# Performance work log

Hardware: AMD Instinct MI355X
Metric: run time of the kernel (lower is better)

The kernel has to match this reference:

```python
import jax, jax.numpy as jnp
import numpy as np

V, E, H, W, S, T, B = 10000, 256, 512, 256, 512, 128, 64


def setup_inputs() -> dict:
    key = jax.random.key(0)
    ks = jax.random.split(key, 17)
    def rn(k, shape, s=0.08):
        return jax.random.normal(k, shape, jnp.float32) * s
    return {
        "tokens": jax.random.randint(ks[0], (B, S), 0, V),
        "dec_h0": jax.random.normal(ks[1], (B, H), jnp.float32),
        "emb_table": rn(ks[2], (V, E), 1.0),
        "enc_Wih": rn(ks[3], (4 * H, E)),
        "enc_Whh": rn(ks[4], (4 * H, H)),
        "enc_bih": rn(ks[5], (4 * H,)),
        "enc_bhh": rn(ks[6], (4 * H,)),
        "dec_Wih": rn(ks[7], (4 * H, E)),
        "dec_Whh": rn(ks[8], (4 * H, H)),
        "dec_bih": rn(ks[9], (4 * H,)),
        "dec_bhh": rn(ks[10], (4 * H,)),
        "W1_w": rn(ks[11], (W, H)),
        "W1_b": rn(ks[12], (W,)),
        "W2_w": rn(ks[13], (W, H)),
        "W2_b": rn(ks[14], (W,)),
        "vt_w": rn(ks[15], (1, W)),
        "vt_b": rn(ks[16], (1,)),
    }


def _lstm_cell(x, h, c, Wih, Whh, bih, bhh):
    # PyTorch gate order: input, forget, cell(g), output
    gates = x @ Wih.T + h @ Whh.T + bih + bhh
    i, f, g, o = jnp.split(gates, 4, axis=-1)
    c = jax.nn.sigmoid(f) * c + jax.nn.sigmoid(i) * jnp.tanh(g)
    h = jax.nn.sigmoid(o) * jnp.tanh(c)
    return h, c


def reference(tokens, dec_h0, emb_table, enc_Wih, enc_Whh, enc_bih, enc_bhh,
              dec_Wih, dec_Whh, dec_bih, dec_bhh, W1_w, W1_b, W2_w, W2_b,
              vt_w, vt_b):
    emb = emb_table[tokens]                       # [B,S,E]
    x_sbe = jnp.swapaxes(emb, 0, 1)               # [S,B,E] time-major
    bsz = tokens.shape[0]
    h0 = jnp.zeros((bsz, enc_Whh.shape[1]), emb.dtype)

    def enc_step(carry, x):
        h, c = carry
        h, c = _lstm_cell(x, h, c, enc_Wih, enc_Whh, enc_bih, enc_bhh)
        return (h, c), h

    _, enc_states = jax.lax.scan(enc_step, (h0, h0), x_sbe)   # [S,B,H]

    # W1(encoder_states) is constant across decoder steps -> hoist it
    blend1 = enc_states @ W1_w.T + W1_b            # [S,B,W]
    c0 = enc_states[-1]                            # original uses last enc state as cell init
    dec_in = jnp.zeros((bsz, emb_table.shape[1]), emb.dtype)  # never updated in original

    def dec_step(carry, _):
        h, c = carry
        h, c = _lstm_cell(dec_in, h, c, dec_Wih, dec_Whh, dec_bih, dec_bhh)
        blend2 = h @ W2_w.T + W2_b                 # [B,W]
        u = (jnp.tanh(blend1 + blend2[None]) @ vt_w.T)[..., 0] + vt_b[0]  # [S,B]
        logp = jax.nn.log_softmax(u.T, axis=1)     # [B,S], softmax over seq positions
        return (h, c), logp

    _, probs = jax.lax.scan(dec_step, (dec_h0, c0), None, length=T)  # [T,B,S]
    return jnp.swapaxes(probs, 0, 1)               # [B,T,S]
```

## Files before the change

### kernel.cpp

```cpp
#include <hip/hip_runtime.h>
#include <hip/hip_bf16.h>
#include <cstdint>
#include <cstddef>

typedef __bf16 bf16_t;
typedef __bf16 bf16x8 __attribute__((ext_vector_type(8)));
typedef float  f32x4  __attribute__((ext_vector_type(4)));

#define NB 64
#define NS 512
#define NTD 128
#define NE 256
#define NH 512
#define NG 2048
#define NW 256

#define HSTEP_DW 16384u

__device__ __forceinline__ float sigm_f(float x) { return 1.f / (1.f + __expf(-x)); }
__device__ __forceinline__ float tanh_f(float x) {
  float e = __expf(2.f * x);
  return 1.f - 2.f / (e + 1.f);
}
__device__ __forceinline__ float bits2f(uint32_t b16) {
  uint32_t u = b16 << 16;
  return __builtin_bit_cast(float, u);
}
__device__ __forceinline__ uint32_t packh(float a, float b) {
  uint16_t lo = __builtin_bit_cast(uint16_t, (bf16_t)a);
  uint16_t hi = __builtin_bit_cast(uint16_t, (bf16_t)b);
  return (uint32_t)lo | ((uint32_t)hi << 16);
}
__device__ __forceinline__ uint32_t aload(const uint32_t* p) {
  return __hip_atomic_load(p, __ATOMIC_RELAXED, __HIP_MEMORY_SCOPE_AGENT);
}
__device__ __forceinline__ uint64_t aload64(const uint64_t* p) {
  return __hip_atomic_load(p, __ATOMIC_RELAXED, __HIP_MEMORY_SCOPE_AGENT);
}
__device__ __forceinline__ void astore(uint32_t* p, uint32_t v) {
  __hip_atomic_store(p, v, __ATOMIC_RELAXED, __HIP_MEMORY_SCOPE_AGENT);
}
__device__ __forceinline__ void astoref(float* p, float v) {
  __hip_atomic_store((uint32_t*)p, __builtin_bit_cast(uint32_t, v),
                     __ATOMIC_RELAXED, __HIP_MEMORY_SCOPE_AGENT);
}
__device__ __forceinline__ float aloadf(const float* p) {
  return __builtin_bit_cast(float, aload((const uint32_t*)p));
}

__global__ __launch_bounds__(256) void pack_b(const float* __restrict__ src,
                                              bf16_t* __restrict__ dst,
                                              int N, int K) {
  int idx = blockIdx.x * 256 + threadIdx.x;
  if (idx >= N * K) return;
  int n = idx / K, k = idx - n * K;
  int lane = (((k & 31) >> 3) << 4) | (n & 15);
  size_t o = ((((size_t)(n >> 4) * (K >> 5)) + (k >> 5)) * 64 + lane) * 8 + (k & 7);
  dst[o] = (bf16_t)src[idx];
}

__global__ __launch_bounds__(256) void gather_emb(const int* __restrict__ tokens,
                                                  const float* __restrict__ table,
                                                  bf16_t* __restrict__ embfrag) {
  int idx = blockIdx.x * 256 + threadIdx.x;
  int row = idx >> 5, e0 = (idx & 31) << 3;
  int b = row & 63, s = row >> 6;
  int tok = tokens[b * NS + s];
  const float4* p = (const float4*)(table + (size_t)tok * NE + e0);
  float4 v0 = p[0], v1 = p[1];
  bf16x8 v;
  v[0] = (bf16_t)v0.x; v[1] = (bf16_t)v0.y; v[2] = (bf16_t)v0.z; v[3] = (bf16_t)v0.w;
  v[4] = (bf16_t)v1.x; v[5] = (bf16_t)v1.y; v[6] = (bf16_t)v1.z; v[7] = (bf16_t)v1.w;
  int mt = row >> 4;
  int ks = e0 >> 5;
  int lane = (b & 15) | (((e0 >> 3) & 3) << 4);
  *(bf16x8*)(embfrag + ((size_t)(mt * 8 + ks) * 64 + lane) * 8) = v;
}

__global__ __launch_bounds__(256) void pack_h0(const float* __restrict__ src,
                                               uint32_t* __restrict__ dst) {
  int idx = blockIdx.x * 256 + threadIdx.x;
  int b = idx >> 8, jp = idx & 255;
  int j = jp * 2;
  float lo = src[(size_t)b * NH + j], hi = src[(size_t)b * NH + j + 1];
  int bg = b >> 4, bl = b & 15, ks = j >> 5;
  int lane = bl | (((j >> 3) & 3) << 4);
  dst[((size_t)bg * 16 + ks) * 256 + lane * 4 + ((j >> 1) & 3)] = packh(lo, hi);
}

template <typename OutT, int KS, int MT>
__global__ __launch_bounds__(256) void gemm_fa2(const bf16_t* __restrict__ A,
                                                const bf16_t* __restrict__ Bp,
                                                OutT* __restrict__ out,
                                                const float* __restrict__ bias1,
                                                const float* __restrict__ bias2,
                                                int N) {
  int lane = threadIdx.x & 63, w = threadIdx.x >> 6;
  int nt = blockIdx.x * 4 + w;
  int mt0 = blockIdx.y * MT;
  bf16x8 bfr[KS];
  const bf16_t* bp = Bp + ((size_t)nt * KS * 64 + lane) * 8;
#pragma unroll
  for (int ks = 0; ks < KS; ++ks) bfr[ks] = *(const bf16x8*)(bp + (size_t)ks * 512);
  int col = (nt << 4) + (lane & 15);
  float bs = bias1[col] + (bias2 ? bias2[col] : 0.f);
  for (int m = 0; m < MT; ++m) {
    int mt = mt0 + m;
    const bf16_t* ap = A + (size_t)mt * (KS * 512) + lane * 8;
    f32x4 acc = {0.f, 0.f, 0.f, 0.f};
#pragma unroll
    for (int ks = 0; ks < KS; ++ks)
      acc = __builtin_amdgcn_mfma_f32_16x16x32_bf16(
          *(const bf16x8*)(ap + (size_t)ks * 512), bfr[ks], acc, 0, 0, 0);
    int rbase = (mt << 4) + ((lane >> 4) << 2);
#pragma unroll
    for (int r = 0; r < 4; ++r)
      out[(size_t)(rbase + r) * N + col] = (OutT)(acc[r] + bs);
  }
}

__global__ __launch_bounds__(256) void enc_chain(
    const bf16_t* __restrict__ Wp, const bf16_t* __restrict__ xih,
    const bf16_t* __restrict__ W1p, const float* __restrict__ W1_b,
    uint32_t* __restrict__ hfrag, uint32_t* __restrict__ flags,
    bf16_t* __restrict__ blend1) {
  __shared__ bf16_t wlds[8 * 8192];
  __shared__ bf16_t w1lds[8192];
  __shared__ float gl[4][16][36];
  const int T = NS;
  int tid = threadIdx.x, lane = tid & 63, wv = tid >> 6;
  int bg = blockIdx.x >> 4, slice = blockIdx.x & 15;

  for (int l = 0; l < 8; ++l) {
    int g = l >> 1, p = l & 1;
    const bf16_t* src = Wp + (size_t)(g * 32 + slice * 2 + p) * 8192;
    bf16_t* dst = wlds + (size_t)l * 8192;
    for (int i = tid; i < 1024; i += 256)
      *(bf16x8*)(dst + (size_t)i * 8) = *(const bf16x8*)(src + (size_t)i * 8);
  }
  {
    const bf16_t* src = W1p + (size_t)slice * 8192;
    for (int i = tid; i < 1024; i += 256)
      *(bf16x8*)(w1lds + (size_t)i * 8) = *(const bf16x8*)(src + (size_t)i * 8);
  }

  int ub = tid >> 4, uj2 = tid & 15;
  int lane_f = ub | ((uj2 >> 2) << 4);
  float c0 = 0.f, c1 = 0.f;
  float b1bias = W1_b[slice * 16 + (lane & 15)];
  __syncthreads();

  const uint64_t* hq = (const uint64_t*)hfrag;
  uint32_t* fl = flags + bg * 16;

  for (int t = 0; t <= T; ++t) {
    uint32_t xd[4];
    if (t < T) {
      const uint32_t* xr = (const uint32_t*)xih +
          ((size_t)(t * 64 + bg * 16 + ub)) * 1024 + slice * 16 + uj2;
#pragma unroll
      for (int g = 0; g < 4; ++g) xd[g] = xr[(size_t)g * 256];
    }
    if (t > 0) {
      if (wv == 0) {
        uint32_t tgt = (uint32_t)t;
        bool ok;
        do {
          uint32_t f = tgt;
          if (lane < 16 && lane != (uint32_t)slice) f = aload(fl + lane);
          ok = __all(f >= tgt);
        } while (!ok);
      }
      __syncthreads();
    }
    const uint64_t* hb = hq + ((size_t)t * 4 + bg) * 2048 + lane * 2;
    uint64_t aq[16][2];
#pragma unroll
    for (int ks = 0; ks < 16; ++ks) {
      aq[ks][0] = aload64(hb + (size_t)ks * 128);
      aq[ks][1] = aload64(hb + (size_t)ks * 128 + 1);
    }
    if (t >= 1 && wv == 0) {
      f32x4 bacc = {0.f, 0.f, 0.f, 0.f};
#pragma unroll
      for (int ks = 0; ks < 16; ++ks) {
        union { uint64_t q[2]; bf16x8 v; } u;
        u.q[0] = aq[ks][0]; u.q[1] = aq[ks][1];
        bacc = __builtin_amdgcn_mfma_f32_16x16x32_bf16(
            u.v, *(const bf16x8*)(w1lds + (size_t)ks * 512 + lane * 8), bacc, 0, 0, 0);
      }
      int col = slice * 16 + (lane & 15);
      int rb = (lane >> 4) << 2;
      size_t rowb = (size_t)(t - 1) * 64 + bg * 16 + rb;
#pragma unroll
      for (int r = 0; r < 4; ++r)
        blend1[(rowb + r) * 256 + col] = (bf16_t)(bacc[r] + b1bias);
    }
    if (t < T) {
      const bf16_t* wl = wlds + (size_t)(wv * 2) * 8192 + lane * 8;
      f32x4 acc0 = {0.f, 0.f, 0.f, 0.f}, acc1 = {0.f, 0.f, 0.f, 0.f};
#pragma unroll
      for (int ks = 0; ks < 16; ++ks) {
        union { uint64_t q[2]; bf16x8 v; } u;
        u.q[0] = aq[ks][0]; u.q[1] = aq[ks][1];
        acc0 = __builtin_amdgcn_mfma_f32_16x16x32_bf16(
            u.v, *(const bf16x8*)(wl + (size_t)ks * 512), acc0, 0, 0, 0);
        acc1 = __builtin_amdgcn_mfma_f32_16x16x32_bf16(
            u.v, *(const bf16x8*)(wl + 8192 + (size_t)ks * 512), acc1, 0, 0, 0);
      }
      int cc = lane & 15, rb = (lane >> 4) << 2;
#pragma unroll
      for (int r = 0; r < 4; ++r) {
        gl[wv][rb + r][cc] = acc0[r];
        gl[wv][rb + r][16 + cc] = acc1[r];
      }
      __syncthreads();
      float p[4][2];
#pragma unroll
      for (int g = 0; g < 4; ++g) {
        p[g][0] = gl[g][ub][uj2 * 2] + bits2f(xd[g] & 0xffffu);
        p[g][1] = gl[g][ub][uj2 * 2 + 1] + bits2f(xd[g] >> 16);
      }
      float i0 = sigm_f(p[0][0]), f0 = sigm_f(p[1][0]);
      float g0 = tanh_f(p[2][0]), o0 = sigm_f(p[3][0]);
      c0 = f0 * c0 + i0 * g0;
      float h0 = o0 * tanh_f(c0);
      float i1 = sigm_f(p[0][1]), f1 = sigm_f(p[1][1]);
      float g1 = tanh_f(p[2][1]), o1 = sigm_f(p[3][1]);
      c1 = f1 * c1 + i1 * g1;
      float h1 = o1 * tanh_f(c1);
      astore(hfrag + ((size_t)(t + 1) * 4 + bg) * 4096 +
                 slice * 256 + lane_f * 4 + (uj2 & 3), packh(h0, h1));
      __syncthreads();
      if (tid == 0) astore(fl + slice, (uint32_t)(t + 1));
    }
  }
}

__global__ __launch_bounds__(256) void dec_attn(
    const bf16_t* __restrict__ Wp, const float* __restrict__ bih,
    const float* __restrict__ bhh, const bf16_t* __restrict__ W2p,
    const float* __restrict__ W2_b, uint32_t* __restrict__ hfrag,
    const uint32_t* __restrict__ c0frag, uint32_t* __restrict__ hflags,
    uint32_t* __restrict__ bl2f, const bf16_t* __restrict__ blend1,
    float* __restrict__ blend2, const float* __restrict__ vt_w,
    float* __restrict__ out) {
  union SM {
    struct { bf16_t wlds[8 * 8192]; bf16_t w2lds[8192]; float gl[4][16][36]; } c;
    struct { float vt[272], b2[272], u[512], red[8]; } a;
  };
  __shared__ SM sm;
  const int T = NTD;
  int tid = threadIdx.x, lane = tid & 63, wv = tid >> 6;

  if (blockIdx.x < 64) {
    int bg = blockIdx.x >> 4, slice = blockIdx.x & 15;
    for (int l = 0; l < 8; ++l) {
      int g = l >> 1, p = l & 1;
      const bf16_t* src = Wp + (size_t)(g * 32 + slice * 2 + p) * 8192;
      bf16_t* dst = sm.c.wlds + (size_t)l * 8192;
      for (int i = tid; i < 1024; i += 256)
        *(bf16x8*)(dst + (size_t)i * 8) = *(const bf16x8*)(src + (size_t)i * 8);
    }
    {
      const bf16_t* src = W2p + (size_t)slice * 8192;
      for (int i = tid; i < 1024; i += 256)
        *(bf16x8*)(sm.c.w2lds + (size_t)i * 8) = *(const bf16x8*)(src + (size_t)i * 8);
    }
    int ub = tid >> 4, uj2 = tid & 15;
    int j_lo = slice * 32 + uj2 * 2;
    int lane_f = ub | ((uj2 >> 2) << 4);
    uint32_t d = c0frag[((size_t)bg * 16 + slice) * 256 + lane_f * 4 + (uj2 & 3)];
    float c0 = bits2f(d & 0xffffu), c1 = bits2f(d >> 16);
    float bsum[4][2];
#pragma unroll
    for (int g = 0; g < 4; ++g) {
      bsum[g][0] = bih[g * NH + j_lo] + bhh[g * NH + j_lo];
      bsum[g][1] = bih[g * NH + j_lo + 1] + bhh[g * NH + j_lo + 1];
    }
    float b2bias = W2_b[slice * 16 + (lane & 15)];
    __syncthreads();

    const uint64_t* hq = (const uint64_t*)hfrag;
    uint32_t* fl = hflags + bg * 16;

    for (int t = 0; t <= T; ++t) {
      if (t > 0) {
        if (wv == 0) {
          uint32_t tgt = (uint32_t)t;
          bool ok;
          do {
            uint32_t f = tgt;
            if (lane < 16 && lane != (uint32_t)slice) f = aload(fl + lane);
            ok = __all(f >= tgt);
          } while (!ok);
        }
        __syncthreads();
      }
      const uint64_t* hb = hq + ((size_t)t * 4 + bg) * 2048 + lane * 2;
      uint64_t aq[16][2];
#pragma unroll
      for (int ks = 0; ks < 16; ++ks) {
        aq[ks][0] = aload64(hb + (size_t)ks * 128);
        aq[ks][1] = aload64(hb + (size_t)ks * 128 + 1);
      }
      if (t >= 1 && wv == 0) {
        f32x4 bacc = {0.f, 0.f, 0.f, 0.f};
#pragma unroll
        for (int ks = 0; ks < 16; ++ks) {
          union { uint64_t q[2]; bf16x8 v; } u;
          u.q[0] = aq[ks][0]; u.q[1] = aq[ks][1];
          bacc = __builtin_amdgcn_mfma_f32_16x16x32_bf16(
              u.v, *(const bf16x8*)(sm.c.w2lds + (size_t)ks * 512 + lane * 8),
              bacc, 0, 0, 0);
        }
        int col = slice * 16 + (lane & 15);
        int rb = (lane >> 4) << 2;
        size_t rowb = (size_t)(t - 1) * 64 + bg * 16 + rb;
#pragma unroll
        for (int r = 0; r < 4; ++r)
          astoref(blend2 + (rowb + r) * 256 + col, bacc[r] + b2bias);
      }
      if (t < T) {
        const bf16_t* wl = sm.c.wlds + (size_t)(wv * 2) * 8192 + lane * 8;
        f32x4 acc0 = {0.f, 0.f, 0.f, 0.f}, acc1 = {0.f, 0.f, 0.f, 0.f};
#pragma unroll
        for (int ks = 0; ks < 16; ++ks) {
          union { uint64_t q[2]; bf16x8 v; } u;
          u.q[0] = aq[ks][0]; u.q[1] = aq[ks][1];
          acc0 = __builtin_amdgcn_mfma_f32_16x16x32_bf16(
              u.v, *(const bf16x8*)(wl + (size_t)ks * 512), acc0, 0, 0, 0);
          acc1 = __builtin_amdgcn_mfma_f32_16x16x32_bf16(
              u.v, *(const bf16x8*)(wl + 8192 + (size_t)ks * 512), acc1, 0, 0, 0);
        }
        int cc = lane & 15, rb = (lane >> 4) << 2;
#pragma unroll
        for (int r = 0; r < 4; ++r) {
          sm.c.gl[wv][rb + r][cc] = acc0[r];
          sm.c.gl[wv][rb + r][16 + cc] = acc1[r];
        }
        __syncthreads();
        float p[4][2];
#pragma unroll
        for (int g = 0; g < 4; ++g) {
          p[g][0] = sm.c.gl[g][ub][uj2 * 2] + bsum[g][0];
          p[g][1] = sm.c.gl[g][ub][uj2 * 2 + 1] + bsum[g][1];
        }
        float i0 = sigm_f(p[0][0]), f0 = sigm_f(p[1][0]);
        float g0 = tanh_f(p[2][0]), o0 = sigm_f(p[3][0]);
        c0 = f0 * c0 + i0 * g0;
        float h0 = o0 * tanh_f(c0);
        float i1 = sigm_f(p[0][1]), f1 = sigm_f(p[1][1]);
        float g1 = tanh_f(p[2][1]), o1 = sigm_f(p[3][1]);
        c1 = f1 * c1 + i1 * g1;
        float h1 = o1 * tanh_f(c1);
        astore(hfrag + ((size_t)(t + 1) * 4 + bg) * 4096 +
                   slice * 256 + lane_f * 4 + (uj2 & 3), packh(h0, h1));
        __syncthreads();
        if (tid == 0) {
          astore(fl + slice, (uint32_t)(t + 1));
          astore(bl2f + bg * 16 + slice, (uint32_t)t);
        }
      } else {
        __syncthreads();
        if (tid == 0) astore(bl2f + bg * 16 + slice, (uint32_t)T);
      }
    }
  } else {
    int w = blockIdx.x - 64;
    for (int k = w; k < NTD * NB; k += 192) {
      int t = k >> 6, b = k & 63;
      if (wv == 0) {
        uint32_t tgt = (uint32_t)(t + 1);
        bool ok;
        do {
          uint32_t f = aload(bl2f + lane);
          ok = __all(f >= tgt);
          if (!ok) __builtin_amdgcn_s_sleep(16);
        } while (!ok);
      }
      __syncthreads();
      {
        int ww = tid;
        int pi = ww + ((ww >> 6) << 2);
        sm.a.vt[pi] = vt_w[ww];
        sm.a.b2[pi] = aloadf(blend2 + (size_t)(t * 64 + b) * NW + ww);
      }
      __syncthreads();
      int wgrp = lane >> 4, sgrp = lane & 15;
      int base = wgrp * 68;
      for (int it = 0; it < 8; ++it) {
        int s = it * 64 + wv * 16 + sgrp;
        const bf16_t* row = blend1 + ((size_t)s * NB + b) * NW + wgrp * 64;
        float val = 0.f;
#pragma unroll
        for (int c8 = 0; c8 < 8; ++c8) {
          bf16x8 v = *(const bf16x8*)(row + c8 * 8);
#pragma unroll
          for (int jx = 0; jx < 8; ++jx) {
            int wi = base + c8 * 8 + jx;
            val += sm.a.vt[wi] * tanh_f((float)v[jx] + sm.a.b2[wi]);
          }
        }
        val += __shfl_xor(val, 16, 64);
        val += __shfl_xor(val, 32, 64);
        if (wgrp == 0) sm.a.u[it * 64 + wv * 16 + sgrp] = val;
      }
      __syncthreads();
      float a = sm.a.u[tid], bb2 = sm.a.u[tid + 256];
      float m = fmaxf(a, bb2);
#pragma unroll
      for (int o = 1; o < 64; o <<= 1) m = fmaxf(m, __shfl_xor(m, o, 64));
      if (lane == 0) sm.a.red[wv] = m;
      __syncthreads();
      m = fmaxf(fmaxf(sm.a.red[0], sm.a.red[1]), fmaxf(sm.a.red[2], sm.a.red[3]));
      float e = __expf(a - m) + __expf(bb2 - m);
#pragma unroll
      for (int o = 1; o < 64; o <<= 1) e += __shfl_xor(e, o, 64);
      if (lane == 0) sm.a.red[4 + wv] = e;
      __syncthreads();
      float lz = m + logf(sm.a.red[4] + sm.a.red[5] + sm.a.red[6] + sm.a.red[7]);
      size_t ob = ((size_t)b * NTD + t) * NS;
      out[ob + tid] = a - lz;
      out[ob + tid + 256] = bb2 - lz;
      __syncthreads();
    }
  }
}

extern "C" void kernel_launch(void* const* d_in, const int* in_sizes, int n_in,
                              void* d_out, int out_size, void* d_ws, size_t ws_size,
                              hipStream_t stream) {
  const int*   tokens    = (const int*)d_in[0];
  const float* dec_h0    = (const float*)d_in[1];
  const float* emb_table = (const float*)d_in[2];
  const float* enc_Wih   = (const float*)d_in[3];
  const float* enc_Whh   = (const float*)d_in[4];
  const float* enc_bih   = (const float*)d_in[5];
  const float* enc_bhh   = (const float*)d_in[6];
  const float* dec_Whh   = (const float*)d_in[8];
  const float* dec_bih   = (const float*)d_in[9];
  const float* dec_bhh   = (const float*)d_in[10];
  const float* W1_w      = (const float*)d_in[11];
  const float* W1_b      = (const float*)d_in[12];
  const float* W2_w      = (const float*)d_in[13];
  const float* W2_b      = (const float*)d_in[14];
  const float* vt_w      = (const float*)d_in[15];
  float* out = (float*)d_out;

  char* w = (char*)d_ws;
  size_t off = 0;
  auto alloc = [&](size_t bytes) {
    size_t o = off;
    off += (bytes + 255) & ~(size_t)255;
    return o;
  };
  bf16_t* embfrag = (bf16_t*)(w + alloc((size_t)NS * NB * NE * 2));
  bf16_t* xih     = (bf16_t*)(w + alloc((size_t)NS * NB * NG * 2));
  uint32_t* enc_hf = (uint32_t*)(w + alloc((size_t)(NS + 1) * HSTEP_DW * 4));
  uint32_t* dec_hf = (uint32_t*)(w + alloc((size_t)(NTD + 1) * HSTEP_DW * 4));
  bf16_t* blend1  = (bf16_t*)(w + alloc((size_t)NS * NB * NW * 2));
  float*  blend2  = (float*)(w + alloc((size_t)NTD * NB * NW * 4));
  bf16_t* pWih    = (bf16_t*)(w + alloc((size_t)NG * NE * 2));
  bf16_t* pWhhE   = (bf16_t*)(w + alloc((size_t)NG * NH * 2));
  bf16_t* pWhhD   = (bf16_t*)(w + alloc((size_t)NG * NH * 2));
  bf16_t* pW1     = (bf16_t*)(w + alloc((size_t)NW * NH * 2));
  bf16_t* pW2     = (bf16_t*)(w + alloc((size_t)NW * NH * 2));
  uint32_t* flags = (uint32_t*)(w + alloc(1024));
  (void)ws_size; (void)in_sizes; (void)n_in; (void)out_size;

  hipMemsetAsync(flags, 0, 768, stream);
  hipMemsetAsync(enc_hf, 0, HSTEP_DW * 4, stream);

  pack_b<<<(NG * NE) / 256, 256, 0, stream>>>(enc_Wih, pWih, NG, NE);
  pack_b<<<(NG * NH) / 256, 256, 0, stream>>>(enc_Whh, pWhhE, NG, NH);
  pack_b<<<(NG * NH) / 256, 256, 0, stream>>>(dec_Whh, pWhhD, NG, NH);
  pack_b<<<(NW * NH) / 256, 256, 0, stream>>>(W1_w, pW1, NW, NH);
  pack_b<<<(NW * NH) / 256, 256, 0, stream>>>(W2_w, pW2, NW, NH);

  gather_emb<<<(NS * NB * (NE / 8)) / 256, 256, 0, stream>>>(tokens, emb_table, embfrag);
  pack_h0<<<64, 256, 0, stream>>>(dec_h0, dec_hf);

  gemm_fa2<bf16_t, 8, 16><<<dim3(128 / 4, 2048 / 16), 256, 0, stream>>>(
      embfrag, pWih, xih, enc_bih, enc_bhh, NG);

  enc_chain<<<64, 256, 0, stream>>>(pWhhE, xih, pW1, W1_b, enc_hf, flags, blend1);

  dec_attn<<<256, 256, 0, stream>>>(pWhhD, dec_bih, dec_bhh, pW2, W2_b, dec_hf,
                                    enc_hf + (size_t)NS * HSTEP_DW, flags + 64,
                                    flags + 128, blend1, blend2, vt_w, out);
}
```

Baseline: 3.243 ms.

## Move W1/W2 projections off the LSTM critical path; use sentinel-based sync

```diff
diff --git a/kernel.cpp b/kernel.cpp
--- a/kernel.cpp
+++ b/kernel.cpp
@@ -16,6 +16,7 @@
 #define NW 256
 
 #define HSTEP_DW 16384u
+#define SENT32 0xFFFFFFFFu
 
 __device__ __forceinline__ float sigm_f(float x) { return 1.f / (1.f + __expf(-x)); }
 __device__ __forceinline__ float tanh_f(float x) {
@@ -43,9 +44,6 @@
 __device__ __forceinline__ void astoref(float* p, float v) {
   __hip_atomic_store((uint32_t*)p, __builtin_bit_cast(uint32_t, v),
                      __ATOMIC_RELAXED, __HIP_MEMORY_SCOPE_AGENT);
-}
-__device__ __forceinline__ float aloadf(const float* p) {
-  return __builtin_bit_cast(float, aload((const uint32_t*)p));
 }
 
 __global__ __launch_bounds__(256) void pack_b(const float* __restrict__ src,
@@ -119,15 +117,11 @@
   }
 }
 
-__global__ __launch_bounds__(256) void enc_chain(
+__global__ __launch_bounds__(256) void lstm_chain_enc(
     const bf16_t* __restrict__ Wp, const bf16_t* __restrict__ xih,
-    const bf16_t* __restrict__ W1p, const float* __restrict__ W1_b,
-    uint32_t* __restrict__ hfrag, uint32_t* __restrict__ flags,
-    bf16_t* __restrict__ blend1) {
+    uint32_t* __restrict__ hfrag, uint32_t* __restrict__ flags) {
   __shared__ bf16_t wlds[8 * 8192];
-  __shared__ bf16_t w1lds[8192];
   __shared__ float gl[4][16][36];
-  const int T = NS;
   int tid = threadIdx.x, lane = tid & 63, wv = tid >> 6;
   int bg = blockIdx.x >> 4, slice = blockIdx.x & 15;
 
@@ -138,31 +132,121 @@
     for (int i = tid; i < 1024; i += 256)
       *(bf16x8*)(dst + (size_t)i * 8) = *(const bf16x8*)(src + (size_t)i * 8);
   }
-  {
-    const bf16_t* src = W1p + (size_t)slice * 8192;
-    for (int i = tid; i < 1024; i += 256)
-      *(bf16x8*)(w1lds + (size_t)i * 8) = *(const bf16x8*)(src + (size_t)i * 8);
-  }
 
   int ub = tid >> 4, uj2 = tid & 15;
   int lane_f = ub | ((uj2 >> 2) << 4);
   float c0 = 0.f, c1 = 0.f;
-  float b1bias = W1_b[slice * 16 + (lane & 15)];
   __syncthreads();
 
   const uint64_t* hq = (const uint64_t*)hfrag;
   uint32_t* fl = flags + bg * 16;
 
-  for (int t = 0; t <= T; ++t) {
+  for (int t = 0; t < NS; ++t) {
     uint32_t xd[4];
-    if (t < T) {
+    {
       const uint32_t* xr = (const uint32_t*)xih +
           ((size_t)(t * 64 + bg * 16 + ub)) * 1024 + slice * 16 + uj2;
 #pragma unroll
       for (int g = 0; g < 4; ++g) xd[g] = xr[(size_t)g * 256];
     }
     if (t > 0) {
-      if (wv == 0) {
+      uint32_t tgt = (uint32_t)t;
+      bool ok;
+      do {
+        uint32_t f = tgt;
+        if (lane < 16 && lane != (uint32_t)slice) f = aload(fl + lane);
+        ok = __all(f >= tgt);
+      } while (!ok);
+    }
+    const uint64_t* hb = hq + ((size_t)t * 4 + bg) * 2048 + lane * 2;
+    uint64_t aq[16][2];
+#pragma unroll
+    for (int ks = 0; ks < 16; ++ks) {
+      aq[ks][0] = aload64(hb + (size_t)ks * 128);
+      aq[ks][1] = aload64(hb + (size_t)ks * 128 + 1);
+    }
+    const bf16_t* wl = wlds + (size_t)(wv * 2) * 8192 + lane * 8;
+    f32x4 acc0 = {0.f, 0.f, 0.f, 0.f}, acc1 = {0.f, 0.f, 0.f, 0.f};
+#pragma unroll
+    for (int ks = 0; ks < 16; ++ks) {
+      union { uint64_t q[2]; bf16x8 v; } u;
+      u.q[0] = aq[ks][0]; u.q[1] = aq[ks][1];
+      acc0 = __builtin_amdgcn_mfma_f32_16x16x32_bf16(
+          u.v, *(const bf16x8*)(wl + (size_t)ks * 512), acc0, 0, 0, 0);
+      acc1 = __builtin_amdgcn_mfma_f32_16x16x32_bf16(
+          u.v, *(const bf16x8*)(wl + 8192 + (size_t)ks * 512), acc1, 0, 0, 0);
+    }
+    int cc = lane & 15, rb = (lane >> 4) << 2;
+#pragma unroll
+    for (int r = 0; r < 4; ++r) {
+      gl[wv][rb + r][cc] = acc0[r];
+      gl[wv][rb + r][16 + cc] = acc1[r];
+    }
+    __syncthreads();
+
+    float p[4][2];
+#pragma unroll
+    for (int g = 0; g < 4; ++g) {
+      p[g][0] = gl[g][ub][uj2 * 2] + bits2f(xd[g] & 0xffffu);
+      p[g][1] = gl[g][ub][uj2 * 2 + 1] + bits2f(xd[g] >> 16);
+    }
+    float i0 = sigm_f(p[0][0]), f0 = sigm_f(p[1][0]);
+    float g0 = tanh_f(p[2][0]), o0 = sigm_f(p[3][0]);
+    c0 = f0 * c0 + i0 * g0;
+    float h0 = o0 * tanh_f(c0);
+    float i1 = sigm_f(p[0][1]), f1 = sigm_f(p[1][1]);
+    float g1 = tanh_f(p[2][1]), o1 = sigm_f(p[3][1]);
+    c1 = f1 * c1 + i1 * g1;
+    float h1 = o1 * tanh_f(c1);
+    astore(hfrag + ((size_t)(t + 1) * 4 + bg) * 4096 +
+               slice * 256 + lane_f * 4 + (uj2 & 3), packh(h0, h1));
+    __syncthreads();
+    if (tid == 0) astore(fl + slice, (uint32_t)(t + 1));
+  }
+}
+
+__global__ __launch_bounds__(256) void dec_fused(
+    const bf16_t* __restrict__ Wp, const float* __restrict__ bih,
+    const float* __restrict__ bhh, const bf16_t* __restrict__ W2p,
+    const float* __restrict__ W2_b, uint32_t* __restrict__ hfrag,
+    const uint32_t* __restrict__ c0frag, uint32_t* __restrict__ flags,
+    const bf16_t* __restrict__ blend1, float* __restrict__ blend2,
+    const float* __restrict__ vt_w, float* __restrict__ out) {
+  union SM {
+    struct { bf16_t wlds[8 * 8192]; float gl[4][16][36]; } c;
+    struct { float vt[272], b2[272], u[512], red[8]; } a;
+  };
+  __shared__ SM sm;
+  int tid = threadIdx.x, lane = tid & 63, wv = tid >> 6;
+  int blk = blockIdx.x;
+
+  if (blk < 64) {
+    int bg = blk >> 4, slice = blk & 15;
+    for (int l = 0; l < 8; ++l) {
+      int g = l >> 1, p = l & 1;
+      const bf16_t* src = Wp + (size_t)(g * 32 + slice * 2 + p) * 8192;
+      bf16_t* dst = sm.c.wlds + (size_t)l * 8192;
+      for (int i = tid; i < 1024; i += 256)
+        *(bf16x8*)(dst + (size_t)i * 8) = *(const bf16x8*)(src + (size_t)i * 8);
+    }
+    int ub = tid >> 4, uj2 = tid & 15;
+    int j_lo = slice * 32 + uj2 * 2;
+    int lane_f = ub | ((uj2 >> 2) << 4);
+    uint32_t d = c0frag[((size_t)bg * 16 + slice) * 256 + lane_f * 4 + (uj2 & 3)];
+    float c0 = bits2f(d & 0xffffu), c1 = bits2f(d >> 16);
+    float bsum[4][2];
+#pragma unroll
+    for (int g = 0; g < 4; ++g) {
+      bsum[g][0] = bih[g * NH + j_lo] + bhh[g * NH + j_lo];
+      bsum[g][1] = bih[g * NH + j_lo + 1] + bhh[g * NH + j_lo + 1];
+    }
+    __syncthreads();
+
+    const uint64_t* hq = (const uint64_t*)hfrag;
+    uint32_t* fl = flags + bg * 16;
+
+    for (int t = 0; t < NTD; ++t) {
+      if (t > 0) {
         uint32_t tgt = (uint32_t)t;
         bool ok;
         do {
@@ -171,33 +255,14 @@
           ok = __all(f >= tgt);
         } while (!ok);
       }
-      __syncthreads();
-    }
-    const uint64_t* hb = hq + ((size_t)t * 4 + bg) * 2048 + lane * 2;
-    uint64_t aq[16][2];
-#pragma unroll
-    for (int ks = 0; ks < 16; ++ks) {
-      aq[ks][0] = aload64(hb + (size_t)ks * 128);
-      aq[ks][1] = aload64(hb + (size_t)ks * 128 + 1);
-    }
-    if (t >= 1 && wv == 0) {
-      f32x4 bacc = {0.f, 0.f, 0.f, 0.f};
+      const uint64_t* hb = hq + ((size_t)t * 4 + bg) * 2048 + lane * 2;
+      uint64_t aq[16][2];
 #pragma unroll
       for (int ks = 0; ks < 16; ++ks) {
-        union { uint64_t q[2]; bf16x8 v; } u;
-        u.q[0] = aq[ks][0]; u.q[1] = aq[ks][1];
-        bacc = __builtin_amdgcn_mfma_f32_16x16x32_bf16(
-            u.v, *(const bf16x8*)(w1lds + (size_t)ks * 512 + lane * 8), bacc, 0, 0, 0);
-      }
-      int col = slice * 16 + (lane & 15);
-      int rb = (lane >> 4) << 2;
-      size_t rowb = (size_t)(t - 1) * 64 + bg * 16 + rb;
-#pragma unroll
-      for (int r = 0; r < 4; ++r)
-        blend1[(rowb + r) * 256 + col] = (bf16_t)(bacc[r] + b1bias);
-    }
-    if (t < T) {
-      const bf16_t* wl = wlds + (size_t)(wv * 2) * 8192 + lane * 8;
+        aq[ks][0] = aload64(hb + (size_t)ks * 128);
+        aq[ks][1] = aload64(hb + (size_t)ks * 128 + 1);
+      }
+      const bf16_t* wl = sm.c.wlds + (size_t)(wv * 2) * 8192 + lane * 8;
       f32x4 acc0 = {0.f, 0.f, 0.f, 0.f}, acc1 = {0.f, 0.f, 0.f, 0.f};
 #pragma unroll
       for (int ks = 0; ks < 16; ++ks) {
@@ -211,15 +276,16 @@
       int cc = lane & 15, rb = (lane >> 4) << 2;
 #pragma unroll
       for (int r = 0; r < 4; ++r) {
-        gl[wv][rb + r][cc] = acc0[r];
-        gl[wv][rb + r][16 + cc] = acc1[r];
-      }
-      __syncthreads();
+        sm.c.gl[wv][rb + r][cc] = acc0[r];
+        sm.c.gl[wv][rb + r][16 + cc] = acc1[r];
+      }
+      __syncthreads();
+
       float p[4][2];
 #pragma unroll
       for (int g = 0; g < 4; ++g) {
-        p[g][0] = gl[g][ub][uj2 * 2] + bits2f(xd[g] & 0xffffu);
-        p[g][1] = gl[g][ub][uj2 * 2 + 1] + bits2f(xd[g] >> 16);
+        p[g][0] = sm.c.gl[g][ub][uj2 * 2] + bsum[g][0];
+        p[g][1] = sm.c.gl[g][ub][uj2 * 2 + 1] + bsum[g][1];
       }
       float i0 = sigm_f(p[0][0]), f0 = sigm_f(p[1][0]);
       float g0 = tanh_f(p[2][0]), o0 = sigm_f(p[3][0]);
@@ -234,157 +300,58 @@
       __syncthreads();
       if (tid == 0) astore(fl + slice, (uint32_t)(t + 1));
     }
-  }
-}
-
-__global__ __launch_bounds__(256) void dec_attn(
-    const bf16_t* __restrict__ Wp, const float* __restrict__ bih,
-    const float* __restrict__ bhh, const bf16_t* __restrict__ W2p,
-    const float* __restrict__ W2_b, uint32_t* __restrict__ hfrag,
-    const uint32_t* __restrict__ c0frag, uint32_t* __restrict__ hflags,
-    uint32_t* __restrict__ bl2f, const bf16_t* __restrict__ blend1,
-    float* __restrict__ blend2, const float* __restrict__ vt_w,
-    float* __restrict__ out) {
-  union SM {
-    struct { bf16_t wlds[8 * 8192]; bf16_t w2lds[8192]; float gl[4][16][36]; } c;
-    struct { float vt[272], b2[272], u[512], red[8]; } a;
-  };
-  __shared__ SM sm;
-  const int T = NTD;
-  int tid = threadIdx.x, lane = tid & 63, wv = tid >> 6;
-
-  if (blockIdx.x < 64) {
-    int bg = blockIdx.x >> 4, slice = blockIdx.x & 15;
-    for (int l = 0; l < 8; ++l) {
-      int g = l >> 1, p = l & 1;
-      const bf16_t* src = Wp + (size_t)(g * 32 + slice * 2 + p) * 8192;
-      bf16_t* dst = sm.c.wlds + (size_t)l * 8192;
-      for (int i = tid; i < 1024; i += 256)
-        *(bf16x8*)(dst + (size_t)i * 8) = *(const bf16x8*)(src + (size_t)i * 8);
-    }
-    {
-      const bf16_t* src = W2p + (size_t)slice * 8192;
-      for (int i = tid; i < 1024; i += 256)
-        *(bf16x8*)(sm.c.w2lds + (size_t)i * 8) = *(const bf16x8*)(src + (size_t)i * 8);
-    }
-    int ub = tid >> 4, uj2 = tid & 15;
-    int j_lo = slice * 32 + uj2 * 2;
-    int lane_f = ub | ((uj2 >> 2) << 4);
-    uint32_t d = c0frag[((size_t)bg * 16 + slice) * 256 + lane_f * 4 + (uj2 & 3)];
-    float c0 = bits2f(d & 0xffffu), c1 = bits2f(d >> 16);
-    float bsum[4][2];
-#pragma unroll
-    for (int g = 0; g < 4; ++g) {
-      bsum[g][0] = bih[g * NH + j_lo] + bhh[g * NH + j_lo];
-      bsum[g][1] = bih[g * NH + j_lo + 1] + bhh[g * NH + j_lo + 1];
-    }
-    float b2bias = W2_b[slice * 16 + (lane & 15)];
-    __syncthreads();
-
+  } else if (blk < 72) {
+    int p = blk - 64;
+    int bg = p >> 1, half = p & 1;
+    int n0 = half * 8 + wv * 2;
+    bf16x8 bf0[16], bf1[16];
+    const bf16_t* bp0 = W2p + ((size_t)n0 * 16 * 64 + lane) * 8;
+    const bf16_t* bp1 = W2p + ((size_t)(n0 + 1) * 16 * 64 + lane) * 8;
+#pragma unroll
+    for (int ks = 0; ks < 16; ++ks) {
+      bf0[ks] = *(const bf16x8*)(bp0 + (size_t)ks * 512);
+      bf1[ks] = *(const bf16x8*)(bp1 + (size_t)ks * 512);
+    }
+    int c = lane & 15, grp = lane >> 4;
+    float bb0 = W2_b[n0 * 16 + c], bb1 = W2_b[(n0 + 1) * 16 + c];
     const uint64_t* hq = (const uint64_t*)hfrag;
-    uint32_t* fl = hflags + bg * 16;
-
-    for (int t = 0; t <= T; ++t) {
-      if (t > 0) {
-        if (wv == 0) {
-          uint32_t tgt = (uint32_t)t;
-          bool ok;
-          do {
-            uint32_t f = tgt;
-            if (lane < 16 && lane != (uint32_t)slice) f = aload(fl + lane);
-            ok = __all(f >= tgt);
-          } while (!ok);
-        }
-        __syncthreads();
-      }
-      const uint64_t* hb = hq + ((size_t)t * 4 + bg) * 2048 + lane * 2;
-      uint64_t aq[16][2];
+    const uint32_t* fl = flags + bg * 16;
+    for (int tt = 1; tt <= NTD; ++tt) {
+      uint32_t tgt = (uint32_t)tt;
+      bool ok;
+      do {
+        uint32_t f = tgt;
+        if (lane < 16) f = aload(fl + lane);
+        ok = __all(f >= tgt);
+      } while (!ok);
+      const uint64_t* hb = hq + ((size_t)tt * 4 + bg) * 2048 + lane * 2;
+      f32x4 a0 = {0.f, 0.f, 0.f, 0.f}, a1 = a0;
 #pragma unroll
       for (int ks = 0; ks < 16; ++ks) {
-        aq[ks][0] = aload64(hb + (size_t)ks * 128);
-        aq[ks][1] = aload64(hb + (size_t)ks * 128 + 1);
-      }
-      if (t >= 1 && wv == 0) {
-        f32x4 bacc = {0.f, 0.f, 0.f, 0.f};
-#pragma unroll
-        for (int ks = 0; ks < 16; ++ks) {
-          union { uint64_t q[2]; bf16x8 v; } u;
-          u.q[0] = aq[ks][0]; u.q[1] = aq[ks][1];
-          bacc = __builtin_amdgcn_mfma_f32_16x16x32_bf16(
-              u.v, *(const bf16x8*)(sm.c.w2lds + (size_t)ks * 512 + lane * 8),
-              bacc, 0, 0, 0);
-        }
-        int col = slice * 16 + (lane & 15);
-        int rb = (lane >> 4) << 2;
-        size_t rowb = (size_t)(t - 1) * 64 + bg * 16 + rb;
-#pragma unroll
-        for (int r = 0; r < 4; ++r)
-          astoref(blend2 + (rowb + r) * 256 + col, bacc[r] + b2bias);
-      }
-      if (t < T) {
-        const bf16_t* wl = sm.c.wlds + (size_t)(wv * 2) * 8192 + lane * 8;
-        f32x4 acc0 = {0.f, 0.f, 0.f, 0.f}, acc1 = {0.f, 0.f, 0.f, 0.f};
-#pragma unroll
-        for (int ks = 0; ks < 16; ++ks) {
-          union { uint64_t q[2]; bf16x8 v; } u;
-          u.q[0] = aq[ks][0]; u.q[1] = aq[ks][1];
-          acc0 = __builtin_amdgcn_mfma_f32_16x16x32_bf16(
-              u.v, *(const bf16x8*)(wl + (size_t)ks * 512), acc0, 0, 0, 0);
-          acc1 = __builtin_amdgcn_mfma_f32_16x16x32_bf16(
-              u.v, *(const bf16x8*)(wl + 8192 + (size_t)ks * 512), acc1, 0, 0, 0);
-        }
-        int cc = lane & 15, rb = (lane >> 4) << 2;
-#pragma unroll
-        for (int r = 0; r < 4; ++r) {
-          sm.c.gl[wv][rb + r][cc] = acc0[r];
-          sm.c.gl[wv][rb + r][16 + cc] = acc1[r];
-        }
-        __syncthreads();
-        float p[4][2];
-#pragma unroll
-        for (int g = 0; g < 4; ++g) {
-          p[g][0] = sm.c.gl[g][ub][uj2 * 2] + bsum[g][0];
-          p[g][1] = sm.c.gl[g][ub][uj2 * 2 + 1] + bsum[g][1];
-        }
-        float i0 = sigm_f(p[0][0]), f0 = sigm_f(p[1][0]);
-        float g0 = tanh_f(p[2][0]), o0 = sigm_f(p[3][0]);
-        c0 = f0 * c0 + i0 * g0;
-        float h0 = o0 * tanh_f(c0);
-        float i1 = sigm_f(p[0][1]), f1 = sigm_f(p[1][1]);
-        float g1 = tanh_f(p[2][1]), o1 = sigm_f(p[3][1]);
-        c1 = f1 * c1 + i1 * g1;
-        float h1 = o1 * tanh_f(c1);
-        astore(hfrag + ((size_t)(t + 1) * 4 + bg) * 4096 +
-                   slice * 256 + lane_f * 4 + (uj2 & 3), packh(h0, h1));
-        __syncthreads();
-        if (tid == 0) {
-          astore(fl + slice, (uint32_t)(t + 1));
-          astore(bl2f + bg * 16 + slice, (uint32_t)t);
-        }
-      } else {
-        __syncthreads();
-        if (tid == 0) astore(bl2f + bg * 16 + slice, (uint32_t)T);
+        union { uint64_t q[2]; bf16x8 v; } u;
+        u.q[0] = aload64(hb + (size_t)ks * 128);
+        u.q[1] = aload64(hb + (size_t)ks * 128 + 1);
+        a0 = __builtin_amdgcn_mfma_f32_16x16x32_bf16(u.v, bf0[ks], a0, 0, 0, 0);
+        a1 = __builtin_amdgcn_mfma_f32_16x16x32_bf16(u.v, bf1[ks], a1, 0, 0, 0);
+      }
+      size_t row = (size_t)(tt - 1) * 64 + bg * 16 + grp * 4;
+#pragma unroll
+      for (int r = 0; r < 4; ++r) {
+        astoref(blend2 + (row + r) * 256 + n0 * 16 + c, a0[r] + bb0);
+        astoref(blend2 + (row + r) * 256 + (n0 + 1) * 16 + c, a1[r] + bb1);
       }
     }
   } else {
-    int w = blockIdx.x - 64;
-    for (int k = w; k < NTD * NB; k += 192) {
+    int w = blk - 72;
+    for (int k = w; k < NTD * NB; k += 184) {
       int t = k >> 6, b = k & 63;
-      if (wv == 0) {
-        uint32_t tgt = (uint32_t)(t + 1);
-        bool ok;
-        do {
-          uint32_t f = aload(bl2f + lane);
-          ok = __all(f >= tgt);
-          if (!ok) __builtin_amdgcn_s_sleep(16);
-        } while (!ok);
-      }
-      __syncthreads();
       {
-        int ww = tid;
-        int pi = ww + ((ww >> 6) << 2);
-        sm.a.vt[pi] = vt_w[ww];
-        sm.a.b2[pi] = aloadf(blend2 + (size_t)(t * 64 + b) * NW + ww);
+        const uint32_t* b2p = (const uint32_t*)blend2 + (size_t)(t * 64 + b) * NW + tid;
+        uint32_t v = aload(b2p);
+        while (v == SENT32) { __builtin_amdgcn_s_sleep(2); v = aload(b2p); }
+        int pi = tid + ((tid >> 6) << 2);
+        sm.a.b2[pi] = __builtin_bit_cast(float, v);
+        sm.a.vt[pi] = vt_w[tid];
       }
       __syncthreads();
       int wgrp = lane >> 4, sgrp = lane & 15;
@@ -466,11 +433,12 @@
   bf16_t* pWhhD   = (bf16_t*)(w + alloc((size_t)NG * NH * 2));
   bf16_t* pW1     = (bf16_t*)(w + alloc((size_t)NW * NH * 2));
   bf16_t* pW2     = (bf16_t*)(w + alloc((size_t)NW * NH * 2));
-  uint32_t* flags = (uint32_t*)(w + alloc(1024));
+  uint32_t* flags = (uint32_t*)(w + alloc(512));
   (void)ws_size; (void)in_sizes; (void)n_in; (void)out_size;
 
-  hipMemsetAsync(flags, 0, 768, stream);
+  hipMemsetAsync(flags, 0, 512, stream);
   hipMemsetAsync(enc_hf, 0, HSTEP_DW * 4, stream);
+  hipMemsetAsync(blend2, 0xFF, (size_t)NTD * NB * NW * 4, stream);
 
   pack_b<<<(NG * NE) / 256, 256, 0, stream>>>(enc_Wih, pWih, NG, NE);
   pack_b<<<(NG * NH) / 256, 256, 0, stream>>>(enc_Whh, pWhhE, NG, NH);
@@ -484,9 +452,12 @@
   gemm_fa2<bf16_t, 8, 16><<<dim3(128 / 4, 2048 / 16), 256, 0, stream>>>(
       embfrag, pWih, xih, enc_bih, enc_bhh, NG);
 
-  enc_chain<<<64, 256, 0, stream>>>(pWhhE, xih, pW1, W1_b, enc_hf, flags, blend1);
-
-  dec_attn<<<256, 256, 0, stream>>>(pWhhD, dec_bih, dec_bhh, pW2, W2_b, dec_hf,
-                                    enc_hf + (size_t)NS * HSTEP_DW, flags + 64,
-                                    flags + 128, blend1, blend2, vt_w, out);
-}
+  lstm_chain_enc<<<64, 256, 0, stream>>>(pWhhE, xih, enc_hf, flags);
+
+  gemm_fa2<bf16_t, 16, 16><<<dim3(16 / 4, 2048 / 16), 256, 0, stream>>>(
+      (const bf16_t*)(enc_hf + HSTEP_DW), pW1, blend1, W1_b, nullptr, NW);
+
+  dec_fused<<<256, 256, 0, stream>>>(pWhhD, dec_bih, dec_bhh, pW2, W2_b,
+                                     dec_hf, enc_hf + (size_t)NS * HSTEP_DW,
+                                     flags + 64, blend1, blend2, vt_w, out);
+}
```

After: 2.998 ms. 7.5% less time.
